# Kernel tuning notes

Measured on AMD Instinct MI355X. Metric: run time of the kernel, lower is better.

## Reference

```python
import jax, jax.numpy as jnp
import numpy as np

N_NODES = 200000
N_EDGES = 600000
NUM_GRAPHS = 8192
IN_CH = 32
HIDDEN = [128, 256]
MLP_HIDDEN = 256
NUM_CLASSES = 10
MAX_SIZE = 40.0
BN_EPS = 1e-5


def setup_inputs() -> dict:
    key = jax.random.key(0)
    ks = jax.random.split(key, 24)
    inp = {}
    inp["x"] = jax.random.normal(ks[0], (N_NODES, IN_CH), dtype=jnp.float32)
    inp["edge_index"] = jax.random.randint(ks[1], (2, N_EDGES), 0, N_NODES, dtype=jnp.int32)
    inp["edge_type"] = jax.random.randint(ks[2], (N_EDGES,), 0, 3, dtype=jnp.int32)
    inp["batch"] = jnp.sort(jax.random.randint(ks[3], (N_NODES,), 0, NUM_GRAPHS, dtype=jnp.int32))
    prev = IN_CH
    ki = 4
    for li, h in enumerate(HIDDEN):
        inp[f"W_conv{li}"] = jax.random.normal(ks[ki], (3, prev, h), dtype=jnp.float32) * (1.0 / np.sqrt(prev)); ki += 1
        inp[f"b_conv{li}"] = jnp.zeros((3, h), dtype=jnp.float32)
        inp[f"W_id{li}"] = jax.random.normal(ks[ki], (prev, h), dtype=jnp.float32) * (1.0 / np.sqrt(prev)); ki += 1
        inp[f"b_id{li}"] = jnp.zeros((h,), dtype=jnp.float32)
        inp[f"gamma{li}"] = jnp.ones((h,), dtype=jnp.float32)
        inp[f"beta{li}"] = jnp.zeros((h,), dtype=jnp.float32)
        prev = h
    inp["W_fc1"] = jax.random.normal(ks[ki], (HIDDEN[-1] + 1, MLP_HIDDEN), dtype=jnp.float32) * (1.0 / np.sqrt(HIDDEN[-1] + 1)); ki += 1
    inp["b_fc1"] = jnp.zeros((MLP_HIDDEN,), dtype=jnp.float32)
    inp["W_fc2"] = jax.random.normal(ks[ki], (MLP_HIDDEN, NUM_CLASSES), dtype=jnp.float32) * (1.0 / np.sqrt(MLP_HIDDEN)); ki += 1
    inp["b_fc2"] = jnp.zeros((NUM_CLASSES,), dtype=jnp.float32)
    return inp


def _gcn_relation(x, W, b, src, dst, w):
    # GCNConv(normalize=True, add_self_loops=False) restricted to edges with weight w in {0,1}
    deg = jax.ops.segment_sum(w, dst, num_segments=N_NODES)          # in-degree of targets
    dinv = jnp.where(deg > 0, 1.0 / jnp.sqrt(jnp.where(deg > 0, deg, 1.0)), 0.0)
    norm = w * dinv[src] * dinv[dst]                                  # [E]
    h = x @ W                                                          # [N, H]
    agg = jax.ops.segment_sum(h[src] * norm[:, None], dst, num_segments=N_NODES)
    return agg + b


def _layer(x, W_conv, b_conv, W_id, b_id, gamma, beta, src, dst, w_rel):
    conv = jax.vmap(lambda W, b, w: _gcn_relation(x, W, b, src, dst, w))(W_conv, b_conv, w_rel)  # [3, N, H]
    out = jnp.sum(jax.nn.relu(conv), axis=0) + jax.nn.relu(x @ W_id + b_id)
    mean = jnp.mean(out, axis=0)
    var = jnp.var(out, axis=0)
    return gamma * (out - mean) / jnp.sqrt(var + BN_EPS) + beta


def reference(x, W_conv0, b_conv0, W_id0, b_id0, gamma0, beta0,
              W_conv1, b_conv1, W_id1, b_id1, gamma1, beta1,
              W_fc1, b_fc1, W_fc2, b_fc2, edge_index, edge_type, batch):
    src, dst = edge_index[0], edge_index[1]
    # one-hot relation weights [3, E]: edge_attr[:, k] == 1 masks
    w_rel = (edge_type[None, :] == jnp.arange(3)[:, None]).astype(x.dtype)
    h = _layer(x, W_conv0, b_conv0, W_id0, b_id0, gamma0, beta0, src, dst, w_rel)
    h = _layer(h, W_conv1, b_conv1, W_id1, b_id1, gamma1, beta1, src, dst, w_rel)
    # global_add_pool
    pooled = jax.ops.segment_sum(h, batch, num_segments=NUM_GRAPHS)   # [G, H]
    counts = jax.ops.segment_sum(jnp.ones((h.shape[0],), h.dtype), batch, num_segments=NUM_GRAPHS)
    pooled = jnp.concatenate([pooled, (counts / MAX_SIZE)[:, None]], axis=1)
    out = jax.nn.relu(pooled @ W_fc1 + b_fc1)
    return out @ W_fc2 + b_fc2
```

## Files before the change

kernel.cpp:

```cpp
#include <hip/hip_runtime.h>
#include <cstdint>
#include <cstddef>

#define NN 200000
#define NE 600000
#define NG 8192
#define C0 32
#define C1 128
#define C2 256
#define MLPH 256
#define NCLS 10
#define NB (3 * NN)
#define SCAN_BPB 1024
#define SCAN_NBLK ((NB + SCAN_BPB - 1) / SCAN_BPB)
#define NREP 8
#define MGB 32

typedef __attribute__((ext_vector_type(8))) short short8b;
typedef __attribute__((ext_vector_type(4))) float f32x4;

__device__ __forceinline__ void atomAddF(float* p, float v) { unsafeAtomicAdd(p, v); }

__device__ __forceinline__ float b2f(unsigned short u) {
  union { unsigned u; float f; } v; v.u = ((unsigned)u) << 16; return v.f;
}
__device__ __forceinline__ unsigned short f2b(float f) {
  union { float f; unsigned u; } v; v.f = f;
  return (unsigned short)((v.u + 0x7FFF + ((v.u >> 16) & 1)) >> 16);
}

__global__ __launch_bounds__(256) void k_fill(float* __restrict__ p, int n, float v) {
  int i = blockIdx.x * 256 + threadIdx.x;
  if (i < n) p[i] = v;
}

__global__ __launch_bounds__(256) void k_counts(const int* __restrict__ batch, float* __restrict__ counts) {
  int n = blockIdx.x * 256 + threadIdx.x;
  if (n < NN) atomAddF(&counts[batch[n]], 1.f);
}

__global__ __launch_bounds__(256) void k_hist(const int* __restrict__ dst, const int* __restrict__ et,
                                              int* __restrict__ cnt) {
  int e = blockIdx.x * 256 + threadIdx.x;
  if (e < NE) atomicAdd(&cnt[et[e] * NN + dst[e]], 1);
}

__global__ __launch_bounds__(256) void k_dinvI(const int* __restrict__ cnt, float* __restrict__ dinv) {
  int i = blockIdx.x * 256 + threadIdx.x;
  if (i < NB) { int c = cnt[i]; dinv[i] = (c > 0) ? 1.f / sqrtf((float)c) : 0.f; }
}

__global__ __launch_bounds__(256) void k_scan1(const int* __restrict__ cnt, int* __restrict__ starts,
                                               int* __restrict__ bsum) {
  __shared__ int sh[256];
  const int b0 = blockIdx.x * SCAN_BPB + threadIdx.x * 4;
  int v[4]; int tot = 0;
#pragma unroll
  for (int j = 0; j < 4; j++) {
    int b = b0 + j;
    v[j] = tot;
    tot += (b < NB) ? cnt[b] : 0;
  }
  sh[threadIdx.x] = tot;
  __syncthreads();
  for (int ofs = 1; ofs < 256; ofs <<= 1) {
    int add = (threadIdx.x >= ofs) ? sh[threadIdx.x - ofs] : 0;
    __syncthreads();
    sh[threadIdx.x] += add;
    __syncthreads();
  }
  const int excl = (threadIdx.x == 0) ? 0 : sh[threadIdx.x - 1];
#pragma unroll
  for (int j = 0; j < 4; j++) {
    int b = b0 + j;
    if (b < NB) starts[b] = excl + v[j];
  }
  if (threadIdx.x == 255) bsum[blockIdx.x] = sh[255];
}

__global__ void k_scan2(int* __restrict__ bsum) {
  if (threadIdx.x == 0) {
    int acc = 0;
    for (int i = 0; i < SCAN_NBLK; i++) { int t = bsum[i]; bsum[i] = acc; acc += t; }
  }
}

__global__ __launch_bounds__(256) void k_scan3(int* __restrict__ starts, const int* __restrict__ bsum) {
  int b = blockIdx.x * 256 + threadIdx.x;
  if (b < NB) starts[b] += bsum[b / SCAN_BPB];
}

__global__ __launch_bounds__(256) void k_place(const int* __restrict__ src, const int* __restrict__ dst,
                                               const int* __restrict__ et, int* __restrict__ starts,
                                               int* __restrict__ esrc) {
  int e = blockIdx.x * 256 + threadIdx.x;
  if (e >= NE) return;
  int b = et[e] * NN + dst[e];
  int pos = atomicAdd(&starts[b], 1);
  esrc[pos] = src[e];
}

__global__ __launch_bounds__(256) void k_prepw(const float* __restrict__ Wid, const float* __restrict__ Wc,
                                               unsigned short* __restrict__ Wtf, int CIN_, int COUT_) {
  int i = blockIdx.x * 256 + threadIdx.x;
  if (i >= 4 * CIN_ * COUT_) return;
  int j = i & 7, lq = (i >> 3) & 63, ct = (i >> 9) & 3;
  int rest = i >> 11;
  int KK = CIN_ / 32, NP = COUT_ / 64;
  int kk = rest % KK; rest /= KK;
  int p = rest % NP; int m = rest / NP;
  int ki = kk * 32 + (lq >> 4) * 4 + (j & 3) + 16 * (j >> 2);
  int c = p * 64 + ct * 16 + (lq & 15);
  float wv = (m == 0) ? Wid[(size_t)ki * COUT_ + c] : Wc[(size_t)((m - 1) * CIN_ + ki) * COUT_ + c];
  Wtf[i] = f2b(wv);
}

template <int CIN, typename TIN>
__global__ __launch_bounds__(256) void k_agg(const int* __restrict__ starts, const int* __restrict__ esrc,
                                             const float* __restrict__ dinv, const TIN* __restrict__ h,
                                             unsigned short* __restrict__ aggXb, int lo, int nloc) {
  constexpr int TPB = (CIN == 32) ? 8 : 16;
  constexpr int V = CIN / TPB;
  const int idx = blockIdx.x * 256 + threadIdx.x;
  const int bl = idx / TPB;
  const int lane = idx % TPB;
  if (bl >= 3 * nloc) return;
  const int t = bl / nloc;
  const int bin = t * NN + lo + (bl - t * nloc);
  const int s = (bin == 0) ? 0 : starts[bin - 1];
  const int e2 = starts[bin];
  float acc[V];
#pragma unroll
  for (int j = 0; j < V; j++) acc[j] = 0.f;
  for (int i = s; i < e2; i++) {
    const int sn = esrc[i];
    const float dv = dinv[(size_t)t * NN + sn];
    if (dv == 0.f) continue;
    const TIN* hp = h + (size_t)sn * CIN + lane * V;
    if constexpr (sizeof(TIN) == 2) {
      ushort4 u0 = *(const ushort4*)hp;
      ushort4 u1 = *(const ushort4*)((const unsigned short*)hp + 4);
      acc[0] = fmaf(b2f(u0.x), dv, acc[0]); acc[1] = fmaf(b2f(u0.y), dv, acc[1]);
      acc[2] = fmaf(b2f(u0.z), dv, acc[2]); acc[3] = fmaf(b2f(u0.w), dv, acc[3]);
      if constexpr (V == 8) {
        acc[4] = fmaf(b2f(u1.x), dv, acc[4]); acc[5] = fmaf(b2f(u1.y), dv, acc[5]);
        acc[6] = fmaf(b2f(u1.z), dv, acc[6]); acc[7] = fmaf(b2f(u1.w), dv, acc[7]);
      }
    } else {
      float4 v0 = *(const float4*)hp;
      acc[0] = fmaf(v0.x, dv, acc[0]); acc[1] = fmaf(v0.y, dv, acc[1]);
      acc[2] = fmaf(v0.z, dv, acc[2]); acc[3] = fmaf(v0.w, dv, acc[3]);
    }
  }
  const float dvd = dinv[bin];
  unsigned short* op = aggXb + (size_t)bl * CIN + lane * V;
  ushort4 o0;
  o0.x = f2b(acc[0] * dvd); o0.y = f2b(acc[1] * dvd);
  o0.z = f2b(acc[2] * dvd); o0.w = f2b(acc[3] * dvd);
  *(ushort4*)op = o0;
  if constexpr (V == 8) {
    ushort4 o1;
    o1.x = f2b(acc[4] * dvd); o1.y = f2b(acc[5] * dvd);
    o1.z = f2b(acc[6] * dvd); o1.w = f2b(acc[7] * dvd);
    *(ushort4*)(op + 4) = o1;
  }
}

#define SLOAD(mm)                                                                        \
  {                                                                                      \
    const short8b* g_ = (const short8b*)Wtf + (size_t)((mm) * NP + p) * PMF;             \
    _Pragma("unroll") for (int ii_ = 0; ii_ < KK; ii_++) wreg[ii_] = g_[ii_ * 256 + tid];\
  }

#define SWRITE(mm)                                                                       \
  {                                                                                      \
    short8b* d_ = wlds + ((mm) & 1) * PMF;                                               \
    _Pragma("unroll") for (int ii_ = 0; ii_ < KK; ii_++) d_[ii_ * 256 + tid] = wreg[ii_];\
  }

#define LOADA_M(A0, A1, mm)                                                              \
  {                                                                                      \
    if constexpr ((mm) > 0) {                                                            \
      const unsigned short* ar_ = aggXb + ((size_t)((mm)-1) * nloc + ln0 + rA) * CIN;    \
      _Pragma("unroll") for (int kk_ = 0; kk_ < KK; kk_++) {                             \
        A0[kk_] = *(const ushort4*)(ar_ + kk_ * 32 + lq * 4);                            \
        A1[kk_] = *(const ushort4*)(ar_ + kk_ * 32 + 16 + lq * 4);                       \
      }                                                                                  \
    } else if constexpr (INBF16) {                                                       \
      const unsigned short* xr_ = (const unsigned short*)Xv + (size_t)nA * CIN;          \
      _Pragma("unroll") for (int kk_ = 0; kk_ < KK; kk_++) {                             \
        A0[kk_] = *(const ushort4*)(xr_ + kk_ * 32 + lq * 4);                            \
        A1[kk_] = *(const ushort4*)(xr_ + kk_ * 32 + 16 + lq * 4);                       \
      }                                                                                  \
    } else {                                                                             \
      const float* xr_ = (const float*)Xv + (size_t)nA * CIN;                            \
      _Pragma("unroll") for (int kk_ = 0; kk_ < KK; kk_++) {                             \
        float4 v0_ = *(const float4*)(xr_ + kk_ * 32 + lq * 4);                          \
        float4 v1_ = *(const float4*)(xr_ + kk_ * 32 + 16 + lq * 4);                     \
        A0[kk_] = make_ushort4(f2b(v0_.x), f2b(v0_.y), f2b(v0_.z), f2b(v0_.w));          \
        A1[kk_] = make_ushort4(f2b(v1_.x), f2b(v1_.y), f2b(v1_.z), f2b(v1_.w));          \
      }                                                                                  \
    }                                                                                    \
  }

#define COMPM(A0, A1, mm)                                                                \
  {                                                                                      \
    f32x4 acc_[4];                                                                       \
    _Pragma("unroll") for (int c_ = 0; c_ < 4; c_++) acc_[c_] = (f32x4){0.f, 0.f, 0.f, 0.f}; \
    const short8b* wb_ = wlds + ((mm) & 1) * PMF;                                        \
    _Pragma("unroll") for (int kk_ = 0; kk_ < KK; kk_++) {                               \
      union { ushort4 u4[2]; short8b v; } fa_;                                           \
      fa_.u4[0] = A0[kk_]; fa_.u4[1] = A1[kk_];                                          \
      _Pragma("unroll") for (int c_ = 0; c_ < 4; c_++)                                   \
          acc_[c_] = __builtin_amdgcn_mfma_f32_16x16x32_bf16(                            \
              fa_.v, wb_[kk_ * 256 + c_ * 64 + l], acc_[c_], 0, 0, 0);                   \
    }                                                                                    \
    const float* bp_ = ((mm) == 0) ? bid : bc + (size_t)((mm)-1) * COUT;                 \
    _Pragma("unroll") for (int c_ = 0; c_ < 4; c_++) {                                   \
      float bb_ = bp_[c0 + c_ * 16 + lr];                                                \
      _Pragma("unroll") for (int j_ = 0; j_ < 4; j_++)                                   \
          run[c_][j_] += fmaxf(acc_[c_][j_] + bb_, 0.f);                                 \
    }                                                                                    \
  }

template <int CIN, int COUT, bool INBF16, bool WRITEOUT, bool DOPOOL>
__global__ __launch_bounds__(256, 3) void k_fin(
    const void* __restrict__ Xv, const unsigned short* __restrict__ aggXb,
    int lo, int nloc, int nt, const unsigned short* __restrict__ Wtf,
    const float* __restrict__ bid, const float* __restrict__ bc,
    unsigned short* __restrict__ outb, float* __restrict__ stats,
    float* __restrict__ pooled, const int* __restrict__ batch) {
  constexpr int NP = COUT / 64;
  constexpr int KK = CIN / 32;
  constexpr int PMF = KK * 256;
  constexpr int EPI = 64 * 65 * 4 + 2 * 4 * 64 * 4 + 64 * 4;
  constexpr int SMEM_BYTES = (2 * PMF * 16 > EPI) ? 2 * PMF * 16 : EPI;
  __shared__ __align__(16) char smem[SMEM_BYTES];
  short8b* wlds = (short8b*)smem;
  float (*tile)[65] = (float(*)[65])smem;
  float* sred = (float*)(smem + 64 * 65 * 4);
  int* sbatch = (int*)(smem + 64 * 65 * 4 + 2 * 4 * 64 * 4);

  const int i = blockIdx.x;
  const int xr8 = i & 7;
  const int xq = i >> 3;
  const int p = xq % NP;
  const int ti = xq / NP;
  const int tileIdx = ti * 8 + xr8;
  if (tileIdx >= nt) return;
  const int ln0 = tileIdx * 64;
  const int n0 = lo + ln0;
  const int c0 = p * 64;
  const int tid = threadIdx.x, w = tid >> 6, l = tid & 63, lr = l & 15, lq = l >> 4;
  const int rA = w * 16 + lr;
  const int nA = n0 + rA;

  f32x4 run[4];
#pragma unroll
  for (int ct = 0; ct < 4; ct++) run[ct] = (f32x4){0.f, 0.f, 0.f, 0.f};

  short8b wreg[KK];
  ushort4 a0A[KK], a1A[KK], a0B[KK], a1B[KK];

  SLOAD(0)
  LOADA_M(a0A, a1A, 0)
  SWRITE(0)
  __syncthreads();
  SLOAD(1)
  LOADA_M(a0B, a1B, 1)
  COMPM(a0A, a1A, 0)
  SWRITE(1)
  __syncthreads();
  SLOAD(2)
  LOADA_M(a0A, a1A, 2)
  COMPM(a0B, a1B, 1)
  SWRITE(2)
  __syncthreads();
  SLOAD(3)
  LOADA_M(a0B, a1B, 3)
  COMPM(a0A, a1A, 2)
  SWRITE(3)
  __syncthreads();
  COMPM(a0B, a1B, 3)
  __syncthreads();

#pragma unroll
  for (int ct = 0; ct < 4; ct++)
#pragma unroll
    for (int j = 0; j < 4; j++) tile[w * 16 + lq * 4 + j][ct * 16 + lr] = run[ct][j];
  if (DOPOOL && tid < 64) sbatch[tid] = batch[n0 + tid];
  __syncthreads();

  if (WRITEOUT) {
    const int r = tid >> 2, cg = (tid & 3) * 16;
    ushort4 o[4];
#pragma unroll
    for (int g4 = 0; g4 < 4; g4++) {
      o[g4].x = f2b(tile[r][cg + g4 * 4 + 0]);
      o[g4].y = f2b(tile[r][cg + g4 * 4 + 1]);
      o[g4].z = f2b(tile[r][cg + g4 * 4 + 2]);
      o[g4].w = f2b(tile[r][cg + g4 * 4 + 3]);
    }
    ushort4* dst4 = (ushort4*)(outb + (size_t)(n0 + r) * COUT + c0 + cg);
#pragma unroll
    for (int g4 = 0; g4 < 4; g4++) dst4[g4] = o[g4];
  }
  {
    const int col = tid & 63, rg = tid >> 6, r0 = rg * 16;
    float s = 0.f, ss = 0.f, gs = 0.f;
    int curg = DOPOOL ? sbatch[r0] : 0;
#pragma unroll
    for (int r = 0; r < 16; r++) {
      float v = tile[r0 + r][col];
      s += v; ss += v * v;
      if (DOPOOL) {
        int g = sbatch[r0 + r];
        if (g != curg) { atomAddF(&pooled[(size_t)curg * C2 + c0 + col], gs); gs = 0.f; curg = g; }
        gs += v;
      }
    }
    if (DOPOOL) atomAddF(&pooled[(size_t)curg * C2 + c0 + col], gs);
    sred[0 * 4 * 64 + rg * 64 + col] = s;
    sred[1 * 4 * 64 + rg * 64 + col] = ss;
  }
  __syncthreads();
  if (tid < 64) {
    float s4 = sred[0 + tid] + sred[64 + tid] + sred[128 + tid] + sred[192 + tid];
    float ss4 = sred[256 + tid] + sred[320 + tid] + sred[384 + tid] + sred[448 + tid];
    float* st = stats + (size_t)(tileIdx & (NREP - 1)) * 2 * COUT;
    atomAddF(&st[c0 + tid], s4);
    atomAddF(&st[COUT + c0 + tid], ss4);
  }
}

__global__ __launch_bounds__(256) void k_bnfin(const float* __restrict__ stats, const float* __restrict__ gamma,
                                               const float* __restrict__ beta, float* __restrict__ sc,
                                               float* __restrict__ sh, int COUT) {
  int c = threadIdx.x;
  if (c < COUT) {
    float su = 0.f, ssu = 0.f;
    for (int r = 0; r < NREP; r++) {
      su += stats[(size_t)r * 2 * COUT + c];
      ssu += stats[(size_t)r * 2 * COUT + COUT + c];
    }
    const float invN = 1.f / (float)NN;
    float m = su * invN;
    float v = ssu * invN - m * m;
    float s = gamma[c] / sqrtf(v + 1e-5f);
    sc[c] = s;
    sh[c] = fmaf(-m, s, beta[c]);
  }
}

__global__ __launch_bounds__(256) void k_bnfold(unsigned short* __restrict__ o, const float* __restrict__ sc,
                                                const float* __restrict__ sh) {
  size_t i8 = ((size_t)blockIdx.x * 256 + threadIdx.x) * 8;
  if (i8 >= (size_t)NN * C1) return;
  const int c = (int)(i8 & (C1 - 1));
  ushort4 a = *(ushort4*)(o + i8);
  ushort4 b = *(ushort4*)(o + i8 + 4);
  a.x = f2b(fmaf(b2f(a.x), sc[c + 0], sh[c + 0]));
  a.y = f2b(fmaf(b2f(a.y), sc[c + 1], sh[c + 1]));
  a.z = f2b(fmaf(b2f(a.z), sc[c + 2], sh[c + 2]));
  a.w = f2b(fmaf(b2f(a.w), sc[c + 3], sh[c + 3]));
  b.x = f2b(fmaf(b2f(b.x), sc[c + 4], sh[c + 4]));
  b.y = f2b(fmaf(b2f(b.y), sc[c + 5], sh[c + 5]));
  b.z = f2b(fmaf(b2f(b.z), sc[c + 6], sh[c + 6]));
  b.w = f2b(fmaf(b2f(b.w), sc[c + 7], sh[c + 7]));
  *(ushort4*)(o + i8) = a;
  *(ushort4*)(o + i8 + 4) = b;
}

__global__ __launch_bounds__(256) void k_mlp(const float* __restrict__ pooled, const float* __restrict__ counts,
                                             const float* __restrict__ sc2, const float* __restrict__ sh2,
                                             const float* __restrict__ Wf1, const float* __restrict__ bf1,
                                             const float* __restrict__ Wf2, const float* __restrict__ bf2,
                                             float* __restrict__ out) {
  __shared__ float featT[257 * 36];
  __shared__ float cnts[MGB];
  const int g0 = blockIdx.x * MGB;
  const int t = threadIdx.x;
  if (t < MGB) cnts[t] = counts[g0 + t];
  __syncthreads();
  {
    const float sc = sc2[t], sh = sh2[t];
    for (int g = 0; g < MGB; g++)
      featT[t * 36 + g] = fmaf(sc, pooled[(size_t)(g0 + g) * C2 + t], sh * cnts[g]);
  }
  if (t < MGB) featT[256 * 36 + t] = cnts[t] * 0.025f;
  __syncthreads();
  float acc[MGB];
  const float b1 = bf1[t];
#pragma unroll
  for (int g = 0; g < MGB; g++) acc[g] = b1;
  for (int i = 0; i < 257; i++) {
    const float wv = Wf1[(size_t)i * MLPH + t];
    const float* fr = &featT[i * 36];
#pragma unroll
    for (int g4 = 0; g4 < MGB / 4; g4++) {
      float4 fg = *(const float4*)(fr + g4 * 4);
      acc[g4 * 4 + 0] = fmaf(fg.x, wv, acc[g4 * 4 + 0]);
      acc[g4 * 4 + 1] = fmaf(fg.y, wv, acc[g4 * 4 + 1]);
      acc[g4 * 4 + 2] = fmaf(fg.z, wv, acc[g4 * 4 + 2]);
      acc[g4 * 4 + 3] = fmaf(fg.w, wv, acc[g4 * 4 + 3]);
    }
  }
  __syncthreads();
  float* hidT = featT;
#pragma unroll
  for (int g = 0; g < MGB; g++) hidT[t * 36 + g] = fmaxf(acc[g], 0.f);
  __syncthreads();
  for (int task = t; task < MGB * NCLS; task += 256) {
    const int g = task / NCLS, c = task % NCLS;
    float o = bf2[c];
    for (int j = 0; j < MLPH; j++) o = fmaf(hidT[j * 36 + g], Wf2[(size_t)j * NCLS + c], o);
    out[(size_t)(g0 + g) * NCLS + c] = o;
  }
}

extern "C" void kernel_launch(void* const* d_in, const int* in_sizes, int n_in,
                              void* d_out, int out_size, void* d_ws, size_t ws_size,
                              hipStream_t stream) {
  const float* x = (const float*)d_in[0];
  const int* ei = (const int*)d_in[1];
  const int* et = (const int*)d_in[2];
  const int* batch = (const int*)d_in[3];
  const float* Wc0 = (const float*)d_in[4];
  const float* bc0 = (const float*)d_in[5];
  const float* Wid0 = (const float*)d_in[6];
  const float* bid0 = (const float*)d_in[7];
  const float* gm0 = (const float*)d_in[8];
  const float* bt0 = (const float*)d_in[9];
  const float* Wc1 = (const float*)d_in[10];
  const float* bc1 = (const float*)d_in[11];
  const float* Wid1 = (const float*)d_in[12];
  const float* bid1 = (const float*)d_in[13];
  const float* gm1 = (const float*)d_in[14];
  const float* bt1 = (const float*)d_in[15];
  const float* Wf1 = (const float*)d_in[16];
  const float* bf1 = (const float*)d_in[17];
  const float* Wf2 = (const float*)d_in[18];
  const float* bf2 = (const float*)d_in[19];
  const int* srcI = ei;
  const int* dstI = ei + NE;
  float* outp = (float*)d_out;

  char* ws = (char*)d_ws;
  size_t off = 0;
  auto take = [&](size_t bytes) -> char* {
    char* p = ws + off;
    off = (off + bytes + 255) & ~(size_t)255;
    return p;
  };
  float* dinv = (float*)take((size_t)NB * 4);
  int* cnt = (int*)take((size_t)NB * 4);
  int* starts = (int*)take((size_t)NB * 4);
  int* bsum = (int*)take((size_t)SCAN_NBLK * 4);
  int* esrc = (int*)take((size_t)NE * 4);
  float* stats1 = (float*)take((size_t)NREP * 2 * C1 * 4);
  float* stats2 = (float*)take((size_t)NREP * 2 * C2 * 4);
  float* sc1 = (float*)take(C1 * 4);
  float* sh1 = (float*)take(C1 * 4);
  float* sc2 = (float*)take(C2 * 4);
  float* sh2 = (float*)take(C2 * 4);
  float* counts = (float*)take((size_t)NG * 4);
  float* pooled = (float*)take((size_t)NG * C2 * 4);
  unsigned short* Wtf1 = (unsigned short*)take((size_t)4 * C0 * C1 * 2);
  unsigned short* Wtf2 = (unsigned short*)take((size_t)4 * C1 * C2 * 2);
  unsigned short* out1 = (unsigned short*)take((size_t)NN * C1 * 2);
  const size_t min_agg = (size_t)3 * 64 * C1 * 2;
  if (off + min_agg > ws_size) {
    k_fill<<<(out_size + 255) / 256, 256, 0, stream>>>(outp, out_size, 100.f);
    return;
  }
  unsigned short* aggXb = (unsigned short*)(ws + off);
  const size_t left = ws_size - off;
  long long ch1 = (long long)(left / ((size_t)3 * C0 * 2)) & ~63LL;
  long long ch2 = (long long)(left / ((size_t)3 * C1 * 2)) & ~63LL;
  if (ch1 > NN) ch1 = NN;
  if (ch2 > NN) ch2 = NN;

  dim3 blk(256);
  hipMemsetAsync(cnt, 0, (size_t)NB * 4, stream);
  hipMemsetAsync(stats1, 0, (size_t)NREP * 2 * C1 * 4, stream);
  hipMemsetAsync(stats2, 0, (size_t)NREP * 2 * C2 * 4, stream);
  hipMemsetAsync(counts, 0, (size_t)NG * 4, stream);
  hipMemsetAsync(pooled, 0, (size_t)NG * C2 * 4, stream);

  k_hist<<<(NE + 255) / 256, blk, 0, stream>>>(dstI, et, cnt);
  k_dinvI<<<(NB + 255) / 256, blk, 0, stream>>>(cnt, dinv);
  k_counts<<<(NN + 255) / 256, blk, 0, stream>>>(batch, counts);
  k_scan1<<<SCAN_NBLK, blk, 0, stream>>>(cnt, starts, bsum);
  k_scan2<<<1, 64, 0, stream>>>(bsum);
  k_scan3<<<(NB + 255) / 256, blk, 0, stream>>>(starts, bsum);
  k_place<<<(NE + 255) / 256, blk, 0, stream>>>(srcI, dstI, et, starts, esrc);

  k_prepw<<<(4 * C0 * C1 + 255) / 256, blk, 0, stream>>>(Wid0, Wc0, Wtf1, C0, C1);
  k_prepw<<<(4 * C1 * C2 + 255) / 256, blk, 0, stream>>>(Wid1, Wc1, Wtf2, C1, C2);

  for (long long lo = 0; lo < NN; lo += ch1) {
    const int nloc = (int)((NN - lo < ch1) ? (NN - lo) : ch1);
    const int nt = nloc / 64;
    const int nt8 = (nt + 7) & ~7;
    k_agg<C0, float><<<(3 * nloc * 8 + 255) / 256, blk, 0, stream>>>(starts, esrc, dinv, x, aggXb,
                                                                     (int)lo, nloc);
    k_fin<C0, C1, false, true, false><<<nt8 * (C1 / 64), blk, 0, stream>>>(
        x, aggXb, (int)lo, nloc, nt, Wtf1, bid0, bc0, out1, stats1, nullptr, nullptr);
  }
  k_bnfin<<<1, blk, 0, stream>>>(stats1, gm0, bt0, sc1, sh1, C1);
  k_bnfold<<<(int)(((size_t)NN * C1 / 8 + 255) / 256), blk, 0, stream>>>(out1, sc1, sh1);

  for (long long lo = 0; lo < NN; lo += ch2) {
    const int nloc = (int)((NN - lo < ch2) ? (NN - lo) : ch2);
    const int nt = nloc / 64;
    const int nt8 = (nt + 7) & ~7;
    k_agg<C1, unsigned short><<<(3 * nloc * 16 + 255) / 256, blk, 0, stream>>>(starts, esrc, dinv, out1,
                                                                               aggXb, (int)lo, nloc);
    k_fin<C1, C2, true, false, true><<<nt8 * (C2 / 64), blk, 0, stream>>>(
        out1, aggXb, (int)lo, nloc, nt, Wtf2, bid1, bc1, nullptr, stats2, pooled, batch);
  }
  k_bnfin<<<1, blk, 0, stream>>>(stats2, gm1, bt1, sc2, sh2, C2);

  k_mlp<<<NG / MGB, blk, 0, stream>>>(pooled, counts, sc2, sh2, Wf1, bf1, Wf2, bf2, outp);
}
```

Measured before the change: 615.7 us.

## Fold BN affine into layer-2 consumers and merge scan/dinv kernels

Removes the standalone batch-norm fold pass over the layer-1 output. The BN scale and shift are now applied on the fly: in the layer-2 aggregation, using a running sum of source dinv values for the shift term, and in the identity-path load of the fused GEMM. Also fuses the dinv computation into the first scan kernel and drops the scan-offset add kernel, so the block offsets are added at use sites in place and agg. This saves a full read-modify-write of the N×128 bf16 activation and several launches, in exchange for extra per-element FMAs and small shared-memory loads in the GEMM prologue.

```diff
diff --git a/kernel.cpp b/kernel.cpp
--- a/kernel.cpp
+++ b/kernel.cpp
@@ -45,21 +45,18 @@
   if (e < NE) atomicAdd(&cnt[et[e] * NN + dst[e]], 1);
 }
 
-__global__ __launch_bounds__(256) void k_dinvI(const int* __restrict__ cnt, float* __restrict__ dinv) {
-  int i = blockIdx.x * 256 + threadIdx.x;
-  if (i < NB) { int c = cnt[i]; dinv[i] = (c > 0) ? 1.f / sqrtf((float)c) : 0.f; }
-}
-
 __global__ __launch_bounds__(256) void k_scan1(const int* __restrict__ cnt, int* __restrict__ starts,
-                                               int* __restrict__ bsum) {
+                                               int* __restrict__ bsum, float* __restrict__ dinv) {
   __shared__ int sh[256];
   const int b0 = blockIdx.x * SCAN_BPB + threadIdx.x * 4;
   int v[4]; int tot = 0;
 #pragma unroll
   for (int j = 0; j < 4; j++) {
     int b = b0 + j;
+    int c = (b < NB) ? cnt[b] : 0;
     v[j] = tot;
-    tot += (b < NB) ? cnt[b] : 0;
+    tot += c;
+    if (b < NB) dinv[b] = (c > 0) ? 1.f / sqrtf((float)c) : 0.f;
   }
   sh[threadIdx.x] = tot;
   __syncthreads();
@@ -85,18 +82,13 @@
   }
 }
 
-__global__ __launch_bounds__(256) void k_scan3(int* __restrict__ starts, const int* __restrict__ bsum) {
-  int b = blockIdx.x * 256 + threadIdx.x;
-  if (b < NB) starts[b] += bsum[b / SCAN_BPB];
-}
-
 __global__ __launch_bounds__(256) void k_place(const int* __restrict__ src, const int* __restrict__ dst,
                                                const int* __restrict__ et, int* __restrict__ starts,
-                                               int* __restrict__ esrc) {
+                                               const int* __restrict__ bsum, int* __restrict__ esrc) {
   int e = blockIdx.x * 256 + threadIdx.x;
   if (e >= NE) return;
   int b = et[e] * NN + dst[e];
-  int pos = atomicAdd(&starts[b], 1);
+  int pos = atomicAdd(&starts[b], 1) + bsum[b >> 10];
   esrc[pos] = src[e];
 }
 
@@ -116,8 +108,10 @@
 }
 
 template <int CIN, typename TIN>
-__global__ __launch_bounds__(256) void k_agg(const int* __restrict__ starts, const int* __restrict__ esrc,
-                                             const float* __restrict__ dinv, const TIN* __restrict__ h,
+__global__ __launch_bounds__(256) void k_agg(const int* __restrict__ starts, const int* __restrict__ bsum,
+                                             const int* __restrict__ esrc, const float* __restrict__ dinv,
+                                             const TIN* __restrict__ h, const float* __restrict__ scin,
+                                             const float* __restrict__ shin,
                                              unsigned short* __restrict__ aggXb, int lo, int nloc) {
   constexpr int TPB = (CIN == 32) ? 8 : 16;
   constexpr int V = CIN / TPB;
@@ -127,15 +121,17 @@
   if (bl >= 3 * nloc) return;
   const int t = bl / nloc;
   const int bin = t * NN + lo + (bl - t * nloc);
-  const int s = (bin == 0) ? 0 : starts[bin - 1];
-  const int e2 = starts[bin];
+  const int s = (bin == 0) ? 0 : starts[bin - 1] + bsum[(bin - 1) >> 10];
+  const int e2 = starts[bin] + bsum[bin >> 10];
   float acc[V];
+  float sdv = 0.f;
 #pragma unroll
   for (int j = 0; j < V; j++) acc[j] = 0.f;
   for (int i = s; i < e2; i++) {
     const int sn = esrc[i];
     const float dv = dinv[(size_t)t * NN + sn];
     if (dv == 0.f) continue;
+    sdv += dv;
     const TIN* hp = h + (size_t)sn * CIN + lane * V;
     if constexpr (sizeof(TIN) == 2) {
       ushort4 u0 = *(const ushort4*)hp;
@@ -154,14 +150,21 @@
   }
   const float dvd = dinv[bin];
   unsigned short* op = aggXb + (size_t)bl * CIN + lane * V;
-  ushort4 o0;
-  o0.x = f2b(acc[0] * dvd); o0.y = f2b(acc[1] * dvd);
-  o0.z = f2b(acc[2] * dvd); o0.w = f2b(acc[3] * dvd);
+  unsigned short ov[V];
+  if (scin) {
+#pragma unroll
+    for (int j = 0; j < V; j++) {
+      const int ch = lane * V + j;
+      ov[j] = f2b(dvd * fmaf(scin[ch], acc[j], shin[ch] * sdv));
+    }
+  } else {
+#pragma unroll
+    for (int j = 0; j < V; j++) ov[j] = f2b(acc[j] * dvd);
+  }
+  ushort4 o0 = make_ushort4(ov[0], ov[1], ov[2], ov[3]);
   *(ushort4*)op = o0;
   if constexpr (V == 8) {
-    ushort4 o1;
-    o1.x = f2b(acc[4] * dvd); o1.y = f2b(acc[5] * dvd);
-    o1.z = f2b(acc[6] * dvd); o1.w = f2b(acc[7] * dvd);
+    ushort4 o1 = make_ushort4(ov[4], ov[5], ov[6], ov[7]);
     *(ushort4*)(op + 4) = o1;
   }
 }
@@ -189,8 +192,24 @@
     } else if constexpr (INBF16) {                                                       \
       const unsigned short* xr_ = (const unsigned short*)Xv + (size_t)nA * CIN;          \
       _Pragma("unroll") for (int kk_ = 0; kk_ < KK; kk_++) {                             \
-        A0[kk_] = *(const ushort4*)(xr_ + kk_ * 32 + lq * 4);                            \
-        A1[kk_] = *(const ushort4*)(xr_ + kk_ * 32 + 16 + lq * 4);                       \
+        ushort4 u0_ = *(const ushort4*)(xr_ + kk_ * 32 + lq * 4);                        \
+        ushort4 u1_ = *(const ushort4*)(xr_ + kk_ * 32 + 16 + lq * 4);                   \
+        if constexpr (AFFINE) {                                                          \
+          const int cb_ = kk_ * 32 + lq * 4;                                             \
+          A0[kk_] = make_ushort4(                                                        \
+              f2b(fmaf(b2f(u0_.x), scs[cb_ + 0], shs[cb_ + 0])),                         \
+              f2b(fmaf(b2f(u0_.y), scs[cb_ + 1], shs[cb_ + 1])),                         \
+              f2b(fmaf(b2f(u0_.z), scs[cb_ + 2], shs[cb_ + 2])),                         \
+              f2b(fmaf(b2f(u0_.w), scs[cb_ + 3], shs[cb_ + 3])));                        \
+          A1[kk_] = make_ushort4(                                                        \
+              f2b(fmaf(b2f(u1_.x), scs[cb_ + 16], shs[cb_ + 16])),                       \
+              f2b(fmaf(b2f(u1_.y), scs[cb_ + 17], shs[cb_ + 17])),                       \
+              f2b(fmaf(b2f(u1_.z), scs[cb_ + 18], shs[cb_ + 18])),                       \
+              f2b(fmaf(b2f(u1_.w), scs[cb_ + 19], shs[cb_ + 19])));                      \
+        } else {                                                                         \
+          A0[kk_] = u0_;                                                                 \
+          A1[kk_] = u1_;                                                                 \
+        }                                                                                \
       }                                                                                  \
     } else {                                                                             \
       const float* xr_ = (const float*)Xv + (size_t)nA * CIN;                            \
@@ -223,10 +242,11 @@
     }                                                                                    \
   }
 
-template <int CIN, int COUT, bool INBF16, bool WRITEOUT, bool DOPOOL>
+template <int CIN, int COUT, bool INBF16, bool AFFINE, bool WRITEOUT, bool DOPOOL>
 __global__ __launch_bounds__(256, 3) void k_fin(
     const void* __restrict__ Xv, const unsigned short* __restrict__ aggXb,
     int lo, int nloc, int nt, const unsigned short* __restrict__ Wtf,
+    const float* __restrict__ scA, const float* __restrict__ shA,
     const float* __restrict__ bid, const float* __restrict__ bc,
     unsigned short* __restrict__ outb, float* __restrict__ stats,
     float* __restrict__ pooled, const int* __restrict__ batch) {
@@ -236,6 +256,8 @@
   constexpr int EPI = 64 * 65 * 4 + 2 * 4 * 64 * 4 + 64 * 4;
   constexpr int SMEM_BYTES = (2 * PMF * 16 > EPI) ? 2 * PMF * 16 : EPI;
   __shared__ __align__(16) char smem[SMEM_BYTES];
+  __shared__ float scs[CIN];
+  __shared__ float shs[CIN];
   short8b* wlds = (short8b*)smem;
   float (*tile)[65] = (float(*)[65])smem;
   float* sred = (float*)(smem + 64 * 65 * 4);
@@ -262,10 +284,14 @@
   short8b wreg[KK];
   ushort4 a0A[KK], a1A[KK], a0B[KK], a1B[KK];
 
+  if constexpr (AFFINE) {
+    for (int c = tid; c < CIN; c += 256) { scs[c] = scA[c]; shs[c] = shA[c]; }
+  }
   SLOAD(0)
-  LOADA_M(a0A, a1A, 0)
+  if constexpr (!AFFINE) { LOADA_M(a0A, a1A, 0) }
   SWRITE(0)
   __syncthreads();
+  if constexpr (AFFINE) { LOADA_M(a0A, a1A, 0) }
   SLOAD(1)
   LOADA_M(a0B, a1B, 1)
   COMPM(a0A, a1A, 0)
@@ -350,25 +376,6 @@
     sc[c] = s;
     sh[c] = fmaf(-m, s, beta[c]);
   }
-}
-
-__global__ __launch_bounds__(256) void k_bnfold(unsigned short* __restrict__ o, const float* __restrict__ sc,
-                                                const float* __restrict__ sh) {
-  size_t i8 = ((size_t)blockIdx.x * 256 + threadIdx.x) * 8;
-  if (i8 >= (size_t)NN * C1) return;
-  const int c = (int)(i8 & (C1 - 1));
-  ushort4 a = *(ushort4*)(o + i8);
-  ushort4 b = *(ushort4*)(o + i8 + 4);
-  a.x = f2b(fmaf(b2f(a.x), sc[c + 0], sh[c + 0]));
-  a.y = f2b(fmaf(b2f(a.y), sc[c + 1], sh[c + 1]));
-  a.z = f2b(fmaf(b2f(a.z), sc[c + 2], sh[c + 2]));
-  a.w = f2b(fmaf(b2f(a.w), sc[c + 3], sh[c + 3]));
-  b.x = f2b(fmaf(b2f(b.x), sc[c + 4], sh[c + 4]));
-  b.y = f2b(fmaf(b2f(b.y), sc[c + 5], sh[c + 5]));
-  b.z = f2b(fmaf(b2f(b.z), sc[c + 6], sh[c + 6]));
-  b.w = f2b(fmaf(b2f(b.w), sc[c + 7], sh[c + 7]));
-  *(ushort4*)(o + i8) = a;
-  *(ushort4*)(o + i8 + 4) = b;
 }
 
 __global__ __launch_bounds__(256) void k_mlp(const float* __restrict__ pooled, const float* __restrict__ counts,
@@ -488,12 +495,10 @@
   hipMemsetAsync(pooled, 0, (size_t)NG * C2 * 4, stream);
 
   k_hist<<<(NE + 255) / 256, blk, 0, stream>>>(dstI, et, cnt);
-  k_dinvI<<<(NB + 255) / 256, blk, 0, stream>>>(cnt, dinv);
   k_counts<<<(NN + 255) / 256, blk, 0, stream>>>(batch, counts);
-  k_scan1<<<SCAN_NBLK, blk, 0, stream>>>(cnt, starts, bsum);
+  k_scan1<<<SCAN_NBLK, blk, 0, stream>>>(cnt, starts, bsum, dinv);
   k_scan2<<<1, 64, 0, stream>>>(bsum);
-  k_scan3<<<(NB + 255) / 256, blk, 0, stream>>>(starts, bsum);
-  k_place<<<(NE + 255) / 256, blk, 0, stream>>>(srcI, dstI, et, starts, esrc);
+  k_place<<<(NE + 255) / 256, blk, 0, stream>>>(srcI, dstI, et, starts, bsum, esrc);
 
   k_prepw<<<(4 * C0 * C1 + 255) / 256, blk, 0, stream>>>(Wid0, Wc0, Wtf1, C0, C1);
   k_prepw<<<(4 * C1 * C2 + 255) / 256, blk, 0, stream>>>(Wid1, Wc1, Wtf2, C1, C2);
@@ -502,22 +507,21 @@
     const int nloc = (int)((NN - lo < ch1) ? (NN - lo) : ch1);
     const int nt = nloc / 64;
     const int nt8 = (nt + 7) & ~7;
-    k_agg<C0, float><<<(3 * nloc * 8 + 255) / 256, blk, 0, stream>>>(starts, esrc, dinv, x, aggXb,
-                                                                     (int)lo, nloc);
-    k_fin<C0, C1, false, true, false><<<nt8 * (C1 / 64), blk, 0, stream>>>(
-        x, aggXb, (int)lo, nloc, nt, Wtf1, bid0, bc0, out1, stats1, nullptr, nullptr);
+    k_agg<C0, float><<<(3 * nloc * 8 + 255) / 256, blk, 0, stream>>>(
+        starts, bsum, esrc, dinv, x, nullptr, nullptr, aggXb, (int)lo, nloc);
+    k_fin<C0, C1, false, false, true, false><<<nt8 * (C1 / 64), blk, 0, stream>>>(
+        x, aggXb, (int)lo, nloc, nt, Wtf1, nullptr, nullptr, bid0, bc0, out1, stats1, nullptr, nullptr);
   }
   k_bnfin<<<1, blk, 0, stream>>>(stats1, gm0, bt0, sc1, sh1, C1);
-  k_bnfold<<<(int)(((size_t)NN * C1 / 8 + 255) / 256), blk, 0, stream>>>(out1, sc1, sh1);
 
   for (long long lo = 0; lo < NN; lo += ch2) {
     const int nloc = (int)((NN - lo < ch2) ? (NN - lo) : ch2);
     const int nt = nloc / 64;
     const int nt8 = (nt + 7) & ~7;
-    k_agg<C1, unsigned short><<<(3 * nloc * 16 + 255) / 256, blk, 0, stream>>>(starts, esrc, dinv, out1,
-                                                                               aggXb, (int)lo, nloc);
-    k_fin<C1, C2, true, false, true><<<nt8 * (C2 / 64), blk, 0, stream>>>(
-        out1, aggXb, (int)lo, nloc, nt, Wtf2, bid1, bc1, nullptr, stats2, pooled, batch);
+    k_agg<C1, unsigned short><<<(3 * nloc * 16 + 255) / 256, blk, 0, stream>>>(
+        starts, bsum, esrc, dinv, out1, sc1, sh1, aggXb, (int)lo, nloc);
+    k_fin<C1, C2, true, true, false, true><<<nt8 * (C2 / 64), blk, 0, stream>>>(
+        out1, aggXb, (int)lo, nloc, nt, Wtf2, sc1, sh1, bid1, bc1, nullptr, stats2, pooled, batch);
   }
   k_bnfin<<<1, blk, 0, stream>>>(stats2, gm1, bt1, sc2, sh2, C2);
 
```

Result: no change. 615.0 us (-0.1%).
